# Performance work log

Hardware: AMD Instinct MI355X
Metric: run time of the kernel (lower is better)

Reference implementation:

```python
import jax, jax.numpy as jnp
import numpy as np

BS = 16
CIN = 32          # input_channels
COUT = 64         # out_channels
OUT_DIM = 1024    # out_dim
S = 2
S0 = 1
K = S * (S0 + 1)  # non-overlapping patch size = 4
D = OUT_DIM * K   # input spatial length = 4096


def setup_inputs() -> dict:
    key = jax.random.key(0)
    k1, k2 = jax.random.split(key)
    x = jax.random.normal(k1, (BS, CIN, D), dtype=jnp.float32)
    # learned parameter, torch.randn init
    weight = jax.random.normal(k2, (COUT, CIN, D), dtype=jnp.float32)
    return {"x": x, "weight": weight}


def reference(x, weight):
    # sharing == 0 path of NonOverlappingLocallyConnected1d:
    #   out[b,o,p] = (1/sqrt(CIN)) * sum_{c,k} x[b,c,p*K+k] * weight[o,c,p*K+k]
    # Original materializes [bs,cout,cin,D] via broadcast multiply then sums
    # over (cin, K); fused here as a single einsum over non-overlapping patches.
    bs = x.shape[0]
    xr = x.reshape(bs, CIN, OUT_DIM, K)        # [b, c, p, k]
    wr = weight.reshape(COUT, CIN, OUT_DIM, K)  # [o, c, p, k]
    out = jnp.einsum('bcpk,ocpk->bop', xr, wr)  # [b, o, p]
    return out / jnp.sqrt(jnp.asarray(CIN, x.dtype))
```

## Files before the change

### kernel.cpp

```cpp
#include <hip/hip_runtime.h>

#define CIN     32
#define COUT    64
#define OUT_DIM 1024
#define RS4     1024

__global__ __launch_bounds__(512, 4) void nolc1d_kernel(
    const float* __restrict__ x,
    const float* __restrict__ w,
    float* __restrict__ out)
{
    const int bid = blockIdx.x;
    const int xcd = bid & 7;
    const int m   = bid >> 3;
    const int og  = m & 3;
    const int pgq = xcd * 32 + (m >> 2);
    const int o0  = og * 16;
    const int pf4 = pgq * 4;

    const int t    = threadIdx.x;
    const int lane = t & 63;
    const int wv   = t >> 6;
    const int cs   = t & 7;
    const int p    = (t >> 3) & 3;
    const int g    = (t >> 5) & 3;
    const int oq   = t >> 7;

    __shared__ float4 wls[2048];
    __shared__ float4 xls[2048];

    const float4* __restrict__ x4 = (const float4*)x;
    const float4* __restrict__ w4 = (const float4*)w;

    {
        const int r = lane >> 2;
        const int q = lane & 3;
        #pragma unroll
        for (int i = 0; i < 4; ++i) {
            const int s  = wv * 4 + i;
            const int rr = s * 16 + r;
            const int hi = rr >> 5;
            const int cc = rr & 31;
            const float4* srcw =
                &w4[((size_t)(o0 + hi) * CIN + cc) * RS4 + pf4 + q];
            __builtin_amdgcn_global_load_lds(
                (const __attribute__((address_space(1))) void*)srcw,
                (__attribute__((address_space(3))) void*)&wls[s * 64],
                16, 0, 0);
            const float4* srcx =
                &x4[((size_t)hi * CIN + cc) * RS4 + pf4 + q];
            __builtin_amdgcn_global_load_lds(
                (const __attribute__((address_space(1))) void*)srcx,
                (__attribute__((address_space(3))) void*)&xls[s * 64],
                16, 0, 0);
        }
    }
    __syncthreads();

    float acc[4][4] = {};
    #pragma unroll 2
    for (int j = 0; j < 4; ++j) {
        const int c = cs + 8 * j;
        float4 xv[4], wq[4];
        #pragma unroll
        for (int bi = 0; bi < 4; ++bi)
            xv[bi] = xls[((g * 4 + bi) * 32 + c) * 4 + p];
        #pragma unroll
        for (int oi = 0; oi < 4; ++oi)
            wq[oi] = wls[((oq * 4 + oi) * 32 + c) * 4 + p];
        #pragma unroll
        for (int bi = 0; bi < 4; ++bi)
            #pragma unroll
            for (int oi = 0; oi < 4; ++oi)
                acc[bi][oi] += xv[bi].x * wq[oi].x + xv[bi].y * wq[oi].y +
                               xv[bi].z * wq[oi].z + xv[bi].w * wq[oi].w;
    }

    #pragma unroll
    for (int d = 1; d <= 4; d <<= 1)
        #pragma unroll
        for (int bi = 0; bi < 4; ++bi)
            #pragma unroll
            for (int oi = 0; oi < 4; ++oi)
                acc[bi][oi] += __shfl_xor(acc[bi][oi], d, 64);

    __syncthreads();
    float* red = (float*)xls;
    const float scale = 0.17677669529663687f;
    if (cs == 0) {
        #pragma unroll
        for (int bi = 0; bi < 4; ++bi)
            #pragma unroll
            for (int oi = 0; oi < 4; ++oi)
                red[((g * 4 + bi) * 16 + (oq * 4 + oi)) * 4 + p] =
                    acc[bi][oi] * scale;
    }
    __syncthreads();

    if (t < 256) {
        const int b  = t >> 4;
        const int ol = t & 15;
        ((float4*)out)[((size_t)b * COUT + o0 + ol) * (OUT_DIM / 4) + pgq] =
            ((float4*)red)[t];
    }
}

extern "C" void kernel_launch(void* const* d_in, const int* in_sizes, int n_in,
                              void* d_out, int out_size, void* d_ws, size_t ws_size,
                              hipStream_t stream) {
    const float* x = (const float*)d_in[0];
    const float* w = (const float*)d_in[1];
    float* out = (float*)d_out;

    nolc1d_kernel<<<dim3(1024), dim3(512), 0, stream>>>(x, w, out);
}
```

Baseline: 86.16 us.

## Double-buffer channel chunks with wider position tiles and direct output stores

Each block now covers 16 patch positions instead of 4 and walks the 32 input channels in four chunks of 8. The chunks are staged into two LDS buffers so the next chunk's global-to-LDS load overlaps compute on the current one. This cuts the grid from 1024 to 256 blocks and replaces the 3-level shuffle plus LDS reduction with a single shuffle and direct global stores. In exchange LDS use doubles, occupancy drops (launch bounds 4 to 2), and 256 blocks may underfill the GPU's CUs.

```diff
diff --git a/kernel.cpp b/kernel.cpp
--- a/kernel.cpp
+++ b/kernel.cpp
@@ -5,7 +5,7 @@
 #define OUT_DIM 1024
 #define RS4     1024
 
-__global__ __launch_bounds__(512, 4) void nolc1d_kernel(
+__global__ __launch_bounds__(512, 2) void nolc1d_kernel(
     const float* __restrict__ x,
     const float* __restrict__ w,
     float* __restrict__ out)
@@ -14,94 +14,92 @@
     const int xcd = bid & 7;
     const int m   = bid >> 3;
     const int og  = m & 3;
-    const int pgq = xcd * 32 + (m >> 2);
+    const int pc  = xcd * 8 + (m >> 2);
     const int o0  = og * 16;
-    const int pf4 = pgq * 4;
+    const int pf0 = pc * 16;
 
     const int t    = threadIdx.x;
     const int lane = t & 63;
     const int wv   = t >> 6;
-    const int cs   = t & 7;
-    const int p    = (t >> 3) & 3;
+    const int p    = t & 15;
+    const int cs   = (t >> 4) & 1;
     const int g    = (t >> 5) & 3;
     const int oq   = t >> 7;
 
-    __shared__ float4 wls[2048];
-    __shared__ float4 xls[2048];
+    __shared__ float4 wls[2][2048];
+    __shared__ float4 xls[2][2048];
 
     const float4* __restrict__ x4 = (const float4*)x;
     const float4* __restrict__ w4 = (const float4*)w;
 
-    {
-        const int r = lane >> 2;
-        const int q = lane & 3;
+    const int r4 = lane >> 4;
+    const int q  = lane & 15;
+
+    auto stage = [&](int buf, int ci) {
         #pragma unroll
         for (int i = 0; i < 4; ++i) {
-            const int s  = wv * 4 + i;
-            const int rr = s * 16 + r;
-            const int hi = rr >> 5;
-            const int cc = rr & 31;
+            const int s   = wv * 4 + i;
+            const int row = s * 4 + r4;
+            const int hi  = row >> 3;
+            const int c   = ci * 8 + (row & 7);
             const float4* srcw =
-                &w4[((size_t)(o0 + hi) * CIN + cc) * RS4 + pf4 + q];
+                &w4[((o0 + hi) * CIN + c) * RS4 + pf0 + q];
             __builtin_amdgcn_global_load_lds(
                 (const __attribute__((address_space(1))) void*)srcw,
-                (__attribute__((address_space(3))) void*)&wls[s * 64],
+                (__attribute__((address_space(3))) void*)&wls[buf][s * 64],
                 16, 0, 0);
             const float4* srcx =
-                &x4[((size_t)hi * CIN + cc) * RS4 + pf4 + q];
+                &x4[(hi * CIN + c) * RS4 + pf0 + q];
             __builtin_amdgcn_global_load_lds(
                 (const __attribute__((address_space(1))) void*)srcx,
-                (__attribute__((address_space(3))) void*)&xls[s * 64],
+                (__attribute__((address_space(3))) void*)&xls[buf][s * 64],
                 16, 0, 0);
         }
-    }
+    };
+
+    float acc[4][4] = {};
+
+    stage(0, 0);
     __syncthreads();
 
-    float acc[4][4] = {};
-    #pragma unroll 2
-    for (int j = 0; j < 4; ++j) {
-        const int c = cs + 8 * j;
-        float4 xv[4], wq[4];
+    #pragma unroll 1
+    for (int ci = 0; ci < 4; ++ci) {
+        if (ci < 3) stage((ci + 1) & 1, ci + 1);
+        const int buf = ci & 1;
         #pragma unroll
-        for (int bi = 0; bi < 4; ++bi)
-            xv[bi] = xls[((g * 4 + bi) * 32 + c) * 4 + p];
-        #pragma unroll
-        for (int oi = 0; oi < 4; ++oi)
-            wq[oi] = wls[((oq * 4 + oi) * 32 + c) * 4 + p];
-        #pragma unroll
-        for (int bi = 0; bi < 4; ++bi)
+        for (int jj = 0; jj < 4; ++jj) {
+            const int cl = cs * 4 + jj;
+            float4 xv[4], wq[4];
+            #pragma unroll
+            for (int bi = 0; bi < 4; ++bi)
+                xv[bi] = xls[buf][((g * 4 + bi) * 8 + cl) * 16 + p];
             #pragma unroll
             for (int oi = 0; oi < 4; ++oi)
-                acc[bi][oi] += xv[bi].x * wq[oi].x + xv[bi].y * wq[oi].y +
-                               xv[bi].z * wq[oi].z + xv[bi].w * wq[oi].w;
+                wq[oi] = wls[buf][((oq * 4 + oi) * 8 + cl) * 16 + p];
+            #pragma unroll
+            for (int bi = 0; bi < 4; ++bi)
+                #pragma unroll
+                for (int oi = 0; oi < 4; ++oi)
+                    acc[bi][oi] += xv[bi].x * wq[oi].x + xv[bi].y * wq[oi].y +
+                                   xv[bi].z * wq[oi].z + xv[bi].w * wq[oi].w;
+        }
+        if (ci < 3) __syncthreads();
     }
 
     #pragma unroll
-    for (int d = 1; d <= 4; d <<= 1)
+    for (int bi = 0; bi < 4; ++bi)
         #pragma unroll
-        for (int bi = 0; bi < 4; ++bi)
-            #pragma unroll
-            for (int oi = 0; oi < 4; ++oi)
-                acc[bi][oi] += __shfl_xor(acc[bi][oi], d, 64);
+        for (int oi = 0; oi < 4; ++oi)
+            acc[bi][oi] += __shfl_xor(acc[bi][oi], 16, 64);
 
-    __syncthreads();
-    float* red = (float*)xls;
     const float scale = 0.17677669529663687f;
     if (cs == 0) {
         #pragma unroll
         for (int bi = 0; bi < 4; ++bi)
             #pragma unroll
             for (int oi = 0; oi < 4; ++oi)
-                red[((g * 4 + bi) * 16 + (oq * 4 + oi)) * 4 + p] =
-                    acc[bi][oi] * scale;
-    }
-    __syncthreads();
-
-    if (t < 256) {
-        const int b  = t >> 4;
-        const int ol = t & 15;
-        ((float4*)out)[((size_t)b * COUT + o0 + ol) * (OUT_DIM / 4) + pgq] =
-            ((float4*)red)[t];
+                out[((size_t)(4 * g + bi) * COUT + o0 + 4 * oq + oi) * OUT_DIM
+                    + pf0 + p] = acc[bi][oi] * scale;
     }
 }
 
@@ -112,5 +110,5 @@
     const float* w = (const float*)d_in[1];
     float* out = (float*)d_out;
 
-    nolc1d_kernel<<<dim3(1024), dim3(512), 0, stream>>>(x, w, out);
+    nolc1d_kernel<<<dim3(256), dim3(512), 0, stream>>>(x, w, out);
 }
```

New measurement: 83.63 us. 1.03x faster.
